# Kernel optimization log

Measured on AMD Instinct MI355X. Metric: run time of the kernel, lower is better.

## Reference

```python
import jax, jax.numpy as jnp
import numpy as np
import math

H = 2048
NH = 16
HD = H // NH  # 128
EPS_LN = 1e-5
RES_SCALE_MAX = 0.3

def _nan_clean(x, lim=10000.0):
    return jnp.nan_to_num(x, nan=0.0, posinf=lim, neginf=-lim)

def setup_inputs() -> dict:
    key = jax.random.key(0)
    ks = jax.random.split(key, 12)
    B, S, T = 4, 2048, 256
    std = 1.0 / math.sqrt(H)
    return {
        "hidden_states": jax.random.normal(ks[0], (B, S, H), jnp.float32),
        "audio_tokens": jax.random.normal(ks[1], (B, T, H), jnp.float32),
        "attention_mask": jax.random.randint(ks[2], (B, T), 0, 2, jnp.int32),
        "Wq": jax.random.normal(ks[3], (H, H), jnp.float32) * std,
        "bq": jnp.zeros((H,), jnp.float32),
        "Wk": jax.random.normal(ks[4], (H, H), jnp.float32) * std,
        "bk": jnp.zeros((H,), jnp.float32),
        "Wv": jax.random.normal(ks[5], (H, H), jnp.float32) * std,
        "bv": jnp.zeros((H,), jnp.float32),
        "Wo": jax.random.normal(ks[6], (H, H), jnp.float32) * std,
        "bo": jnp.zeros((H,), jnp.float32),
        "ln_gamma": jnp.ones((H,), jnp.float32),
        "ln_beta": jnp.zeros((H,), jnp.float32),
        "residual_scale": jnp.float32(0.05),
    }

def reference(hidden_states, audio_tokens, attention_mask,
              Wq, bq, Wk, bk, Wv, bv, Wo, bo, ln_gamma, ln_beta, residual_scale):
    B, S, _ = hidden_states.shape
    T = audio_tokens.shape[1]
    hs = _nan_clean(hidden_states).astype(jnp.float32)
    at = _nan_clean(audio_tokens).astype(jnp.float32)
    # Q/K/V projections -> (B, heads, len, head_dim)
    def proj(x, W, b, L):
        y = x @ W.T + b
        return y.reshape(B, L, NH, HD).transpose(0, 2, 1, 3)
    q = _nan_clean(proj(hs, Wq, bq, S))
    k = _nan_clean(proj(at, Wk, bk, T))
    v = _nan_clean(proj(at, Wv, bv, T))
    scale = max(math.sqrt(HD), 1e-8)
    scores = jnp.einsum('bhsd,bhtd->bhst', q, k) / scale
    scores = jnp.clip(scores, -50.0, 50.0)
    scores = jnp.nan_to_num(scores, nan=0.0, posinf=50.0, neginf=-50.0)
    # mask: int 0/1 -> attend where > 0.5, broadcast (B,1,1,T)
    attend = (attention_mask.astype(jnp.float32) > 0.5)[:, None, None, :]
    scores = jnp.where(attend, scores, -10000.0)
    scores = jnp.clip(scores, -50.0, 50.0)
    probs = jax.nn.softmax(scores, axis=-1)
    probs = jnp.nan_to_num(probs, nan=0.0, posinf=1.0, neginf=0.0)
    probs = probs / (probs.sum(axis=-1, keepdims=True) + 1e-8)
    # dropout: eval mode -> identity
    ctx = jnp.einsum('bhst,bhtd->bhsd', probs, v)
    ctx = ctx.transpose(0, 2, 1, 3).reshape(B, S, H)
    delta = _nan_clean(ctx @ Wo.T + bo)
    rs = jnp.clip(residual_scale, 0.0, RES_SCALE_MAX)
    delta = rs * delta
    # LayerNorm (biased variance, like torch)
    mu = delta.mean(axis=-1, keepdims=True)
    var = jnp.mean((delta - mu) ** 2, axis=-1, keepdims=True)
    delta = (delta - mu) / jnp.sqrt(var + EPS_LN) * ln_gamma + ln_beta
    return delta
```

## Files before the change

kernel.cpp:

```cpp
#include <hip/hip_runtime.h>
#include <stdint.h>

typedef unsigned short u16;
typedef __attribute__((ext_vector_type(8))) __bf16 bf16x8;
typedef __attribute__((ext_vector_type(4))) float f32x4;

#define AS1 __attribute__((address_space(1)))
#define AS3 __attribute__((address_space(3)))

constexpr int HB = 4;
constexpr int SS = 2048;
constexpr int TT = 256;
constexpr int HH = 2048;
constexpr int NHEAD = 16;
constexpr int HD = 128;

__device__ __forceinline__ u16 f2b(float f) {
  union { float f; uint32_t u; } c; c.f = f;
  return (u16)((c.u + 0x7FFFu + ((c.u >> 16) & 1u)) >> 16);
}

__device__ __forceinline__ float b2f(uint32_t lo16) {
  union { uint32_t u; float f; } c; c.u = lo16 << 16;
  return c.f;
}

__global__ __launch_bounds__(256)
void cast_all(const float* __restrict__ hs, const float* __restrict__ at,
              const float* __restrict__ wq, const float* __restrict__ wk,
              const float* __restrict__ wv, const float* __restrict__ wo,
              u16* __restrict__ o_hs, u16* __restrict__ o_at,
              u16* __restrict__ o_wq, u16* __restrict__ o_wk,
              u16* __restrict__ o_wv, u16* __restrict__ o_wo) {
  const int b = blockIdx.x;
  const float* src; u16* dst; int base;
  if (b < 16384)      { src = hs; dst = o_hs; base = 0; }
  else if (b < 18432) { src = at; dst = o_at; base = 16384; }
  else if (b < 22528) { src = wq; dst = o_wq; base = 18432; }
  else if (b < 26624) { src = wk; dst = o_wk; base = 22528; }
  else if (b < 30720) { src = wv; dst = o_wv; base = 26624; }
  else                { src = wo; dst = o_wo; base = 30720; }
  const size_t i = (size_t)(b - base) * 256 + threadIdx.x;
  const float4 v = *(const float4*)(src + i * 4);
  uint2 pk;
  pk.x = (uint32_t)f2b(v.x) | ((uint32_t)f2b(v.y) << 16);
  pk.y = (uint32_t)f2b(v.z) | ((uint32_t)f2b(v.w) << 16);
  *(uint2*)(dst + i * 4) = pk;
}

template<int MODE>
__global__ __launch_bounds__(512, 2)
void gemm8(const u16* __restrict__ A, const u16* __restrict__ Bw,
           const float* __restrict__ bias, const float* __restrict__ rsp,
           void* __restrict__ outp) {
  constexpr int KD = 2048, NT = 64;
  constexpr int BUF = 16384;
  __shared__ u16 lds[4 * BUF];
  const int tid = threadIdx.x;
  const int wv = tid >> 6, ln = tid & 63;
  const int lq = ln >> 4, lr = ln & 15;
  const int wm = wv >> 2, wn = wv & 3;

  const int linb = blockIdx.y * 8 + blockIdx.x;
  const int ns = (linb & 7) * 32 + (linb >> 3);
  const int m0 = (ns >> 3) * 256;
  const int n0 = (ns & 7) * 256;

  int gOff[2];
#pragma unroll
  for (int c = 0; c < 2; ++c) {
    const int g = c * 512 + tid, sr = g >> 3, s = g & 7, l = s ^ (sr & 7);
    gOff[c] = (2 * sr + (l >> 2)) * KD + (l & 3) * 8;
  }
  const u16* Abase = A + (size_t)m0 * KD;
  const u16* Bbase = Bw + (size_t)n0 * KD;

  int aoff[8], boff[4];
#pragma unroll
  for (int m = 0; m < 8; ++m) {
    const int R = wm * 128 + m * 16 + lr, sr = R >> 1;
    aoff[m] = sr * 64 + ((((R & 1) << 2) + lq) ^ (sr & 7)) * 8;
  }
#pragma unroll
  for (int j = 0; j < 4; ++j) {
    const int R = wn * 64 + j * 16 + lr, sr = R >> 1;
    boff[j] = 8192 + sr * 64 + ((((R & 1) << 2) + lq) ^ (sr & 7)) * 8;
  }

#define STAGE_A(c, k0, buf)                                                      \
  __builtin_amdgcn_global_load_lds((AS1 const void*)(Abase + (k0) + gOff[c]),    \
      (AS3 void*)(lds + (buf) * BUF + ((c) * 512 + wv * 64) * 8), 16, 0, 0)
#define STAGE_B(c, k0, buf)                                                      \
  __builtin_amdgcn_global_load_lds((AS1 const void*)(Bbase + (k0) + gOff[c]),    \
      (AS3 void*)(lds + (buf) * BUF + 8192 + ((c) * 512 + wv * 64) * 8), 16, 0, 0)

  f32x4 acc[8][4];
#pragma unroll
  for (int i = 0; i < 8; ++i)
#pragma unroll
    for (int j = 0; j < 4; ++j) acc[i][j] = (f32x4){0.f, 0.f, 0.f, 0.f};

  STAGE_A(0, 0, 0);  STAGE_A(1, 0, 0);  STAGE_B(0, 0, 0);  STAGE_B(1, 0, 0);
  STAGE_A(0, 32, 1); STAGE_A(1, 32, 1); STAGE_B(0, 32, 1); STAGE_B(1, 32, 1);
  STAGE_A(0, 64, 2); STAGE_A(1, 64, 2); STAGE_B(0, 64, 2); STAGE_B(1, 64, 2);
  asm volatile("s_waitcnt vmcnt(8)" ::: "memory");
  __builtin_amdgcn_s_barrier();
  __builtin_amdgcn_sched_barrier(0);

  bf16x8 af[4], bf[4], afn[4];
#pragma unroll
  for (int j = 0; j < 4; ++j) bf[j] = *(const bf16x8*)(lds + boff[j]);
#pragma unroll
  for (int m = 0; m < 4; ++m) af[m] = *(const bf16x8*)(lds + aoff[m]);
  __builtin_amdgcn_sched_barrier(0);

  for (int t = 0; t < NT; ++t) {
    const u16* bb = lds + (t & 3) * BUF;
    const u16* bn = lds + ((t + 1) & 3) * BUF;
    const int stg = (t + 3) & 3;
    const int k3 = (t + 3) * 32;
    const bool doStage = (t + 3) < NT;

#pragma unroll
    for (int m = 0; m < 4; ++m) afn[m] = *(const bf16x8*)(bb + aoff[4 + m]);
    if (doStage) { STAGE_A(0, k3, stg); STAGE_A(1, k3, stg); }
    asm volatile("s_waitcnt lgkmcnt(4)" ::: "memory");
    __builtin_amdgcn_sched_barrier(0);
    __builtin_amdgcn_s_setprio(1);
#pragma unroll
    for (int m = 0; m < 4; ++m)
#pragma unroll
      for (int j = 0; j < 4; ++j)
        acc[m][j] = __builtin_amdgcn_mfma_f32_16x16x32_bf16(af[m], bf[j], acc[m][j], 0, 0, 0);
    __builtin_amdgcn_s_setprio(0);
    if (doStage) { STAGE_B(0, k3, stg); STAGE_B(1, k3, stg); }
    if (t < NT - 3)       asm volatile("s_waitcnt vmcnt(8)" ::: "memory");
    else if (t == NT - 3) asm volatile("s_waitcnt vmcnt(4)" ::: "memory");
    else                  asm volatile("s_waitcnt vmcnt(0)" ::: "memory");
    asm volatile("s_waitcnt lgkmcnt(0)" ::: "memory");
    __builtin_amdgcn_s_barrier();
    __builtin_amdgcn_sched_barrier(0);
    if (t + 1 < NT) {
#pragma unroll
      for (int m = 0; m < 4; ++m) af[m] = *(const bf16x8*)(bn + aoff[m]);
    }
    __builtin_amdgcn_s_setprio(1);
#pragma unroll
    for (int m = 0; m < 4; ++m)
#pragma unroll
      for (int j = 0; j < 4; ++j)
        acc[4 + m][j] = __builtin_amdgcn_mfma_f32_16x16x32_bf16(afn[m], bf[j], acc[4 + m][j], 0, 0, 0);
    __builtin_amdgcn_s_setprio(0);
    if (t + 1 < NT) {
#pragma unroll
      for (int j = 0; j < 4; ++j) bf[j] = *(const bf16x8*)(bn + boff[j]);
    }
    __builtin_amdgcn_sched_barrier(0);
  }
#undef STAGE_A
#undef STAGE_B

  float bj[4];
#pragma unroll
  for (int j = 0; j < 4; ++j) bj[j] = bias[n0 + wn * 64 + j * 16 + lr];
  float rsv = 0.f;
  if constexpr (MODE == 2 || MODE == 3) rsv = fminf(fmaxf(rsp[0], 0.0f), 0.3f);

#pragma unroll
  for (int i = 0; i < 8; ++i)
#pragma unroll
    for (int j = 0; j < 4; ++j)
#pragma unroll
      for (int r = 0; r < 4; ++r) {
        const int row = m0 + wm * 128 + i * 16 + lq * 4 + r;
        const int col = n0 + wn * 64 + j * 16 + lr;
        const float v = acc[i][j][r] + bj[j];
        if constexpr (MODE == 0) {
          ((u16*)outp)[(size_t)row * 2048 + col] = f2b(v);
        } else if constexpr (MODE == 2) {
          ((float*)outp)[(size_t)row * 2048 + col] = v * rsv;
        } else {
          ((u16*)outp)[(size_t)row * 2048 + col] = f2b(v * rsv);
        }
      }
}

__global__ __launch_bounds__(256, 2)
void gemm_kv(const u16* __restrict__ A, const u16* __restrict__ Wk,
             const u16* __restrict__ Wv, const float* __restrict__ bkp,
             const float* __restrict__ bvp, u16* __restrict__ Ko,
             u16* __restrict__ Vto) {
  constexpr int KD = 2048, NT = 64;
  constexpr int BUFE = 8192;
  __shared__ u16 lds[4 * BUFE];
  const bool isV = blockIdx.z != 0;
  const u16* Bw = isV ? Wv : Wk;
  const float* bias = isV ? bvp : bkp;
  const int tid = threadIdx.x;
  const int wave = tid >> 6, lane = tid & 63;
  const int lq = lane >> 4, lr = lane & 15;
  const int wr = wave >> 1, wc = wave & 1;
  const int m0 = blockIdx.y * 128, n0 = blockIdx.x * 128;

  int gOff[2];
#pragma unroll
  for (int c = 0; c < 2; ++c) {
    const int g = c * 256 + tid, sr = g >> 3, s = g & 7, l = s ^ (sr & 7);
    gOff[c] = (2 * sr + (l >> 2)) * KD + (l & 3) * 8;
  }
  const u16* Abase = A + (size_t)m0 * KD;
  const u16* Bbase = Bw + (size_t)n0 * KD;

  int aoff[4], boff[4];
#pragma unroll
  for (int i = 0; i < 4; ++i) {
    const int R = wr * 64 + i * 16 + lr, sr = R >> 1;
    aoff[i] = sr * 64 + ((((R & 1) << 2) + lq) ^ (sr & 7)) * 8;
  }
#pragma unroll
  for (int j = 0; j < 4; ++j) {
    const int R = wc * 64 + j * 16 + lr, sr = R >> 1;
    boff[j] = 4096 + sr * 64 + ((((R & 1) << 2) + lq) ^ (sr & 7)) * 8;
  }

#define KV_STAGE(t3, buf)                                                         \
  {                                                                               \
    _Pragma("unroll")                                                             \
    for (int c_ = 0; c_ < 2; ++c_) {                                              \
      __builtin_amdgcn_global_load_lds(                                           \
          (AS1 const void*)(Abase + (t3) * 32 + gOff[c_]),                        \
          (AS3 void*)(lds + (buf) * BUFE + (c_ * 256 + wave * 64) * 8), 16, 0, 0);\
      __builtin_amdgcn_global_load_lds(                                           \
          (AS1 const void*)(Bbase + (t3) * 32 + gOff[c_]),                        \
          (AS3 void*)(lds + (buf) * BUFE + 4096 + (c_ * 256 + wave * 64) * 8),    \
          16, 0, 0);                                                              \
    }                                                                             \
  }

  f32x4 acc[4][4];
#pragma unroll
  for (int i = 0; i < 4; ++i)
#pragma unroll
    for (int j = 0; j < 4; ++j) acc[i][j] = (f32x4){0.f, 0.f, 0.f, 0.f};

  KV_STAGE(0, 0); KV_STAGE(1, 1); KV_STAGE(2, 2);
  asm volatile("s_waitcnt vmcnt(8)" ::: "memory");
  __builtin_amdgcn_s_barrier();
  __builtin_amdgcn_sched_barrier(0);

  bf16x8 af[4], bfr[4];
#pragma unroll
  for (int i = 0; i < 4; ++i) af[i] = *(const bf16x8*)(lds + aoff[i]);
#pragma unroll
  for (int j = 0; j < 4; ++j) bfr[j] = *(const bf16x8*)(lds + boff[j]);
  __builtin_amdgcn_sched_barrier(0);

  for (int t = 0; t < NT; ++t) {
    if (t + 3 < NT) KV_STAGE(t + 3, (t + 3) & 3);
    asm volatile("s_waitcnt lgkmcnt(0)" ::: "memory");
    __builtin_amdgcn_sched_barrier(0);
    __builtin_amdgcn_s_setprio(1);
#pragma unroll
    for (int i = 0; i < 4; ++i)
#pragma unroll
      for (int j = 0; j < 4; ++j)
        acc[i][j] = __builtin_amdgcn_mfma_f32_16x16x32_bf16(af[i], bfr[j], acc[i][j], 0, 0, 0);
    __builtin_amdgcn_s_setprio(0);
    if (t < NT - 3)       asm volatile("s_waitcnt vmcnt(8)" ::: "memory");
    else if (t == NT - 3) asm volatile("s_waitcnt vmcnt(4)" ::: "memory");
    else                  asm volatile("s_waitcnt vmcnt(0)" ::: "memory");
    __builtin_amdgcn_s_barrier();
    __builtin_amdgcn_sched_barrier(0);
    if (t + 1 < NT) {
      const u16* bn = lds + ((t + 1) & 3) * BUFE;
#pragma unroll
      for (int i = 0; i < 4; ++i) af[i] = *(const bf16x8*)(bn + aoff[i]);
#pragma unroll
      for (int j = 0; j < 4; ++j) bfr[j] = *(const bf16x8*)(bn + boff[j]);
    }
    __builtin_amdgcn_sched_barrier(0);
  }
#undef KV_STAGE

  float bj[4];
#pragma unroll
  for (int j = 0; j < 4; ++j) bj[j] = bias[n0 + wc * 64 + j * 16 + lr];

#pragma unroll
  for (int i = 0; i < 4; ++i)
#pragma unroll
    for (int j = 0; j < 4; ++j)
#pragma unroll
      for (int r = 0; r < 4; ++r) {
        const int row = m0 + wr * 64 + i * 16 + lq * 4 + r;
        const int col = n0 + wc * 64 + j * 16 + lr;
        const float v = acc[i][j][r] + bj[j];
        if (!isV) {
          Ko[(size_t)row * 2048 + col] = f2b(v);
        } else {
          Vto[(size_t)(row >> 8) * (2048 * 256) + (size_t)col * 256 + (row & 255)] = f2b(v);
        }
      }
}

__global__ __launch_bounds__(512, 4)
void attn_kernel(const u16* __restrict__ Q, const u16* __restrict__ Kb,
                 const u16* __restrict__ Vt, const int* __restrict__ mask,
                 u16* __restrict__ ctx) {
  __shared__ u16 sK[2][64 * 128];
  __shared__ u16 sVt[2][128 * 64];
  __shared__ u16 sP[8 * 16 * 64];

  const int tid = threadIdx.x;
  const int wv = tid >> 6, ln = tid & 63;
  const int lq = ln >> 4, lr = ln & 15;
  const int h = blockIdx.y, b = blockIdx.z;
  const int s0blk = blockIdx.x * 128;
  u16* sPw = sP + wv * (16 * 64);

  uint32_t mbits = 0;
#pragma unroll
  for (int g = 0; g < 16; ++g)
    mbits |= (mask[b * TT + g * 16 + lr] != 0 ? 1u : 0u) << g;

  bf16x8 qf[4];
  {
    const u16* qp = Q + ((size_t)b * SS + s0blk + wv * 16 + lr) * HH + (size_t)h * HD + lq * 8;
#pragma unroll
    for (int kd = 0; kd < 4; ++kd) qf[kd] = *(const bf16x8*)(qp + kd * 32);
  }

#define STAGE_KV(c)                                                                      \
  {                                                                                      \
    const int buf_ = (c) & 1;                                                            \
    _Pragma("unroll")                                                                    \
    for (int it = 0; it < 2; ++it) {                                                     \
      const int ub = it * 512 + wv * 64;                                                 \
      const int u = ub + ln;                                                             \
      const int row = u >> 4, slot = u & 15, src = slot ^ (row & 15);                    \
      const u16* g = Kb + ((size_t)b * TT + (c) * 64 + row) * HH + h * HD + src * 8;     \
      __builtin_amdgcn_global_load_lds((AS1 const void*)g,                               \
          (AS3 void*)(sK[buf_] + (size_t)ub * 8), 16, 0, 0);                             \
    }                                                                                    \
    _Pragma("unroll")                                                                    \
    for (int it = 0; it < 2; ++it) {                                                     \
      const int ub = it * 512 + wv * 64;                                                 \
      const int u = ub + ln;                                                             \
      const int row = u >> 3, slot = u & 7, src = slot ^ (row & 7);                      \
      const u16* g = Vt + ((size_t)b * HH + h * HD + row) * TT + (c) * 64 + src * 8;     \
      __builtin_amdgcn_global_load_lds((AS1 const void*)g,                               \
          (AS3 void*)(sVt[buf_] + (size_t)ub * 8), 16, 0, 0);                            \
    }                                                                                    \
  }
  STAGE_KV(0);
  STAGE_KV(1);

  const float scale = 0.08838834764831845f;
  float ls[4] = {0.f, 0.f, 0.f, 0.f};
  f32x4 o[8];
#pragma unroll
  for (int d0 = 0; d0 < 8; ++d0) o[d0] = (f32x4){0.f, 0.f, 0.f, 0.f};

  const int qrow = wv * 16 + lr;
  const int shsrc = ((lr >> 2) << 4) + lr;

  for (int c = 0; c < 4; ++c) {
    const int buf = c & 1;
    if (c < 3) asm volatile("s_waitcnt vmcnt(4)" ::: "memory");
    else       asm volatile("s_waitcnt vmcnt(0)" ::: "memory");
    __syncthreads();

    f32x4 sc[4];
#pragma unroll
    for (int tt = 0; tt < 4; ++tt) {
      f32x4 a = (f32x4){0.f, 0.f, 0.f, 0.f};
#pragma unroll
      for (int kd = 0; kd < 4; ++kd) {
        bf16x8 kf = *(const bf16x8*)(sK[buf] + (size_t)(tt * 16 + lr) * 128 + (size_t)((kd * 4 + lq) ^ lr) * 8);
        a = __builtin_amdgcn_mfma_f32_16x16x32_bf16(qf[kd], kf, a, 0, 0, 0);
      }
      sc[tt] = a;
    }

#pragma unroll
    for (int tt = 0; tt < 4; ++tt) {
      const bool on = (mbits >> (c * 4 + tt)) & 1;
#pragma unroll
      for (int r = 0; r < 4; ++r) {
        float v = sc[tt][r] * scale;
        v = fminf(fmaxf(v, -50.f), 50.f);
        v = on ? v : -50.f;
        const float p = __expf(v);
        sc[tt][r] = p;
        ls[r] += p;
      }
    }

#pragma unroll
    for (int tt = 0; tt < 4; ++tt)
#pragma unroll
      for (int r = 0; r < 4; ++r) {
        const int q = lq * 4 + r;
        const int slot = (tt * 2 + (lr >> 3)) ^ ((q >> 1) & 7);
        sPw[(size_t)q * 64 + slot * 8 + (lr & 7)] = f2b(sc[tt][r]);
      }

    bf16x8 pf[2];
#pragma unroll
    for (int kt = 0; kt < 2; ++kt) {
      const int slot = (kt * 4 + lq) ^ ((lr >> 1) & 7);
      pf[kt] = *(const bf16x8*)(sPw + (size_t)lr * 64 + slot * 8);
    }

#pragma unroll
    for (int d0 = 0; d0 < 8; ++d0)
#pragma unroll
      for (int kt = 0; kt < 2; ++kt) {
        bf16x8 vf = *(const bf16x8*)(sVt[buf] + (size_t)(d0 * 16 + lr) * 64 + (size_t)((kt * 4 + lq) ^ (lr & 7)) * 8);
        o[d0] = __builtin_amdgcn_mfma_f32_16x16x32_bf16(vf, pf[kt], o[d0], 0, 0, 0);
      }
    if (c < 2) {
      __syncthreads();
      STAGE_KV(c + 2);
    }
  }
#undef STAGE_KV

#pragma unroll
  for (int d = 1; d < 16; d <<= 1)
#pragma unroll
    for (int r = 0; r < 4; ++r) ls[r] += __shfl_xor(ls[r], d);

  const float i0 = __shfl(1.0f / ls[0], shsrc), i1 = __shfl(1.0f / ls[1], shsrc);
  const float i2 = __shfl(1.0f / ls[2], shsrc), i3 = __shfl(1.0f / ls[3], shsrc);
  const int rsel = lr & 3;
  const float iq = rsel == 0 ? i0 : rsel == 1 ? i1 : rsel == 2 ? i2 : i3;

  const size_t cbase = ((size_t)b * SS + s0blk + wv * 16 + lr) * HH + (size_t)h * HD;
#pragma unroll
  for (int d0 = 0; d0 < 8; ++d0) {
    uint2 w;
    w.x = (uint32_t)f2b(o[d0][0] * iq) | ((uint32_t)f2b(o[d0][1] * iq) << 16);
    w.y = (uint32_t)f2b(o[d0][2] * iq) | ((uint32_t)f2b(o[d0][3] * iq) << 16);
    *(uint2*)(ctx + cbase + d0 * 16 + lq * 4) = w;
  }
}

__global__ __launch_bounds__(256)
void ln_kernel(const u16* __restrict__ in, float* __restrict__ out,
               const float* __restrict__ gamma, const float* __restrict__ beta) {
  const int row = blockIdx.x, tid = threadIdx.x;
  const u16* x = in + (size_t)row * 2048;
  const uint4 raw = *(const uint4*)(x + tid * 8);
  float xv[8];
  xv[0] = b2f(raw.x & 0xFFFFu); xv[1] = b2f(raw.x >> 16);
  xv[2] = b2f(raw.y & 0xFFFFu); xv[3] = b2f(raw.y >> 16);
  xv[4] = b2f(raw.z & 0xFFFFu); xv[5] = b2f(raw.z >> 16);
  xv[6] = b2f(raw.w & 0xFFFFu); xv[7] = b2f(raw.w >> 16);
  float s = 0.f, ss = 0.f;
#pragma unroll
  for (int i = 0; i < 8; ++i) { s += xv[i]; ss += xv[i] * xv[i]; }
#pragma unroll
  for (int d = 1; d < 64; d <<= 1) {
    s += __shfl_xor(s, d);
    ss += __shfl_xor(ss, d);
  }
  __shared__ float rbuf[8];
  const int w = tid >> 6;
  if ((tid & 63) == 0) { rbuf[w] = s; rbuf[4 + w] = ss; }
  __syncthreads();
  s = rbuf[0] + rbuf[1] + rbuf[2] + rbuf[3];
  ss = rbuf[4] + rbuf[5] + rbuf[6] + rbuf[7];
  const float mu = s * (1.0f / 2048.0f);
  const float var = ss * (1.0f / 2048.0f) - mu * mu;
  const float inv = rsqrtf(var + 1e-5f);
  const float4 g0 = *(const float4*)(gamma + tid * 8);
  const float4 g1 = *(const float4*)(gamma + tid * 8 + 4);
  const float4 b0 = *(const float4*)(beta + tid * 8);
  const float4 b1 = *(const float4*)(beta + tid * 8 + 4);
  float4 y0, y1;
  y0.x = (xv[0] - mu) * inv * g0.x + b0.x;
  y0.y = (xv[1] - mu) * inv * g0.y + b0.y;
  y0.z = (xv[2] - mu) * inv * g0.z + b0.z;
  y0.w = (xv[3] - mu) * inv * g0.w + b0.w;
  y1.x = (xv[4] - mu) * inv * g1.x + b1.x;
  y1.y = (xv[5] - mu) * inv * g1.y + b1.y;
  y1.z = (xv[6] - mu) * inv * g1.z + b1.z;
  y1.w = (xv[7] - mu) * inv * g1.w + b1.w;
  float* o = out + (size_t)row * 2048 + tid * 8;
  *(float4*)o = y0;
  *(float4*)(o + 4) = y1;
}

extern "C" void kernel_launch(void* const* d_in, const int* in_sizes, int n_in,
                              void* d_out, int out_size, void* d_ws, size_t ws_size,
                              hipStream_t stream) {
  (void)in_sizes; (void)n_in; (void)out_size; (void)ws_size;
  const float* hs = (const float*)d_in[0];
  const float* at = (const float*)d_in[1];
  const int* mask = (const int*)d_in[2];
  const float* Wq = (const float*)d_in[3];
  const float* bq = (const float*)d_in[4];
  const float* Wk = (const float*)d_in[5];
  const float* bk = (const float*)d_in[6];
  const float* Wv = (const float*)d_in[7];
  const float* bv = (const float*)d_in[8];
  const float* Wo = (const float*)d_in[9];
  const float* bo = (const float*)d_in[10];
  const float* lg = (const float*)d_in[11];
  const float* lb = (const float*)d_in[12];
  const float* rs = (const float*)d_in[13];

  u16* hs_bf = (u16*)d_ws;
  u16* at_bf = hs_bf + 16777216;
  u16* Wq_bf = at_bf + 2097152;
  u16* Wk_bf = Wq_bf + 4194304;
  u16* Wv_bf = Wk_bf + 4194304;
  u16* Wo_bf = Wv_bf + 4194304;
  u16* Q_bf  = Wo_bf + 4194304;
  u16* K_bf  = Q_bf + 16777216;
  u16* Vt_bf = K_bf + 2097152;
  u16* ctx_bf = hs_bf;
  u16* delta_bf = Q_bf;

  cast_all<<<34816, 256, 0, stream>>>(hs, at, Wq, Wk, Wv, Wo,
                                      hs_bf, at_bf, Wq_bf, Wk_bf, Wv_bf, Wo_bf);

  gemm8<0><<<dim3(8, 32), 512, 0, stream>>>(hs_bf, Wq_bf, bq, nullptr, Q_bf);
  gemm_kv<<<dim3(16, 8, 2), 256, 0, stream>>>(at_bf, Wk_bf, Wv_bf, bk, bv, K_bf, Vt_bf);

  attn_kernel<<<dim3(16, 16, 4), 512, 0, stream>>>(Q_bf, K_bf, Vt_bf, mask, ctx_bf);

  gemm8<3><<<dim3(8, 32), 512, 0, stream>>>(ctx_bf, Wo_bf, bo, rs, delta_bf);
  ln_kernel<<<8192, 256, 0, stream>>>(delta_bf, (float*)d_out, lg, lb);
}
```

Before: 248.8 us.

## Restructure GEMM main loop with double-buffered B fragments and post-barrier staging

Rewrites the bf16 MFMA GEMM inner loop as a two-way unrolled SLICE macro. B fragments now live in two register sets (bf/bfn), so the next tile's B and A loads from LDS are interleaved between the two MFMA halves. All four global-to-LDS stage loads for tile t+3 are now issued together after the barrier. The loop now does a full vmcnt(0) wait every iteration, which shortens how far global prefetch runs ahead. The two-way unroll also assumes the K-tile count NT is even.

```diff
diff --git a/kernel.cpp b/kernel.cpp
--- a/kernel.cpp
+++ b/kernel.cpp
@@ -103,60 +103,72 @@
   STAGE_A(0, 0, 0);  STAGE_A(1, 0, 0);  STAGE_B(0, 0, 0);  STAGE_B(1, 0, 0);
   STAGE_A(0, 32, 1); STAGE_A(1, 32, 1); STAGE_B(0, 32, 1); STAGE_B(1, 32, 1);
   STAGE_A(0, 64, 2); STAGE_A(1, 64, 2); STAGE_B(0, 64, 2); STAGE_B(1, 64, 2);
-  asm volatile("s_waitcnt vmcnt(8)" ::: "memory");
+  asm volatile("s_waitcnt vmcnt(4)" ::: "memory");
   __builtin_amdgcn_s_barrier();
   __builtin_amdgcn_sched_barrier(0);
 
-  bf16x8 af[4], bf[4], afn[4];
+  bf16x8 af[4], afn[4], bf[4], bfn[4];
 #pragma unroll
   for (int j = 0; j < 4; ++j) bf[j] = *(const bf16x8*)(lds + boff[j]);
 #pragma unroll
   for (int m = 0; m < 4; ++m) af[m] = *(const bf16x8*)(lds + aoff[m]);
+#pragma unroll
+  for (int m = 0; m < 4; ++m) afn[m] = *(const bf16x8*)(lds + aoff[4 + m]);
   __builtin_amdgcn_sched_barrier(0);
 
-  for (int t = 0; t < NT; ++t) {
-    const u16* bb = lds + (t & 3) * BUF;
-    const u16* bn = lds + ((t + 1) & 3) * BUF;
-    const int stg = (t + 3) & 3;
-    const int k3 = (t + 3) * 32;
-    const bool doStage = (t + 3) < NT;
-
-#pragma unroll
-    for (int m = 0; m < 4; ++m) afn[m] = *(const bf16x8*)(bb + aoff[4 + m]);
-    if (doStage) { STAGE_A(0, k3, stg); STAGE_A(1, k3, stg); }
-    asm volatile("s_waitcnt lgkmcnt(4)" ::: "memory");
-    __builtin_amdgcn_sched_barrier(0);
-    __builtin_amdgcn_s_setprio(1);
-#pragma unroll
-    for (int m = 0; m < 4; ++m)
-#pragma unroll
-      for (int j = 0; j < 4; ++j)
-        acc[m][j] = __builtin_amdgcn_mfma_f32_16x16x32_bf16(af[m], bf[j], acc[m][j], 0, 0, 0);
-    __builtin_amdgcn_s_setprio(0);
-    if (doStage) { STAGE_B(0, k3, stg); STAGE_B(1, k3, stg); }
-    if (t < NT - 3)       asm volatile("s_waitcnt vmcnt(8)" ::: "memory");
-    else if (t == NT - 3) asm volatile("s_waitcnt vmcnt(4)" ::: "memory");
-    else                  asm volatile("s_waitcnt vmcnt(0)" ::: "memory");
-    asm volatile("s_waitcnt lgkmcnt(0)" ::: "memory");
-    __builtin_amdgcn_s_barrier();
-    __builtin_amdgcn_sched_barrier(0);
-    if (t + 1 < NT) {
-#pragma unroll
-      for (int m = 0; m < 4; ++m) af[m] = *(const bf16x8*)(bn + aoff[m]);
-    }
-    __builtin_amdgcn_s_setprio(1);
-#pragma unroll
-    for (int m = 0; m < 4; ++m)
-#pragma unroll
-      for (int j = 0; j < 4; ++j)
-        acc[4 + m][j] = __builtin_amdgcn_mfma_f32_16x16x32_bf16(afn[m], bf[j], acc[4 + m][j], 0, 0, 0);
-    __builtin_amdgcn_s_setprio(0);
-    if (t + 1 < NT) {
-#pragma unroll
-      for (int j = 0; j < 4; ++j) bf[j] = *(const bf16x8*)(bn + boff[j]);
-    }
-    __builtin_amdgcn_sched_barrier(0);
-  }
+#define SLICE(t, A0, A1, BC, BN)                                                 \
+  {                                                                              \
+    const bool nx = (t) + 1 < NT;                                                \
+    const u16* nb = lds + (((t) + 1) & 3) * BUF;                                 \
+    if (nx) {                                                                    \
+      _Pragma("unroll")                                                          \
+      for (int j = 0; j < 4; ++j) BN[j] = *(const bf16x8*)(nb + boff[j]);        \
+    }                                                                            \
+    __builtin_amdgcn_sched_barrier(0);                                           \
+    __builtin_amdgcn_s_setprio(1);                                               \
+    _Pragma("unroll")                                                            \
+    for (int m = 0; m < 4; ++m)                                                  \
+      _Pragma("unroll")                                                          \
+      for (int j = 0; j < 4; ++j)                                                \
+        acc[m][j] = __builtin_amdgcn_mfma_f32_16x16x32_bf16(A0[m], BC[j], acc[m][j], 0, 0, 0); \
+    __builtin_amdgcn_s_setprio(0);                                               \
+    __builtin_amdgcn_sched_barrier(0);                                           \
+    if (nx) {                                                                    \
+      _Pragma("unroll")                                                          \
+      for (int m = 0; m < 4; ++m) A0[m] = *(const bf16x8*)(nb + aoff[m]);        \
+    }                                                                            \
+    __builtin_amdgcn_sched_barrier(0);                                           \
+    __builtin_amdgcn_s_setprio(1);                                               \
+    _Pragma("unroll")                                                            \
+    for (int m = 0; m < 4; ++m)                                                  \
+      _Pragma("unroll")                                                          \
+      for (int j = 0; j < 4; ++j)                                                \
+        acc[4 + m][j] = __builtin_amdgcn_mfma_f32_16x16x32_bf16(A1[m], BC[j], acc[4 + m][j], 0, 0, 0); \
+    __builtin_amdgcn_s_setprio(0);                                               \
+    __builtin_amdgcn_sched_barrier(0);                                           \
+    if (nx) {                                                                    \
+      _Pragma("unroll")                                                          \
+      for (int m = 0; m < 4; ++m) A1[m] = *(const bf16x8*)(nb + aoff[4 + m]);    \
+      asm volatile("s_waitcnt lgkmcnt(4)" ::: "memory");      \
+    } else {                                                                     \
+      asm volatile("s_waitcnt lgkmcnt(0)" ::: "memory");                         \
+    }                                                                            \
+    asm volatile("s_waitcnt vmcnt(0)" ::: "memory");      \
+    __builtin_amdgcn_s_barrier();                                                \
+    __builtin_amdgcn_sched_barrier(0);                                           \
+    if ((t) + 3 < NT) {                                                          \
+      const int k3 = ((t) + 3) * 32, sb = ((t) + 3) & 3;                         \
+      STAGE_A(0, k3, sb); STAGE_A(1, k3, sb);                                    \
+      STAGE_B(0, k3, sb); STAGE_B(1, k3, sb);                                    \
+    }                                                                            \
+    __builtin_amdgcn_sched_barrier(0);                                           \
+  }
+
+  for (int t = 0; t < NT; t += 2) {
+    SLICE(t, af, afn, bf, bfn);
+    SLICE(t + 1, af, afn, bfn, bf);
+  }
+#undef SLICE
 #undef STAGE_A
 #undef STAGE_B
 
```

After: 258.2 us. 1.04x slower.

## Shrink Q/O projection GEMM tiles to 128x128 with 4-wave blocks

Applied to the files above, without the earlier changes.

The large Q and output-projection GEMMs move from 256x256 tiles on 8-wave blocks to 128x128 tiles on 4-wave blocks, giving 1024 workgroups instead of 256. The split A-fragment double-issue schedule is replaced by a simpler single MFMA phase per k-step, with combined A/B staging. The aim is more blocks for better CU occupancy and load balance on MI355X. The cost is lower arithmetic intensity per tile (more global/LDS traffic per FLOP) and less intra-iteration overlap of LDS reads with MFMA.

```diff
diff --git a/kernel.cpp b/kernel.cpp
--- a/kernel.cpp
+++ b/kernel.cpp
@@ -49,131 +49,117 @@
 }
 
 template<int MODE>
-__global__ __launch_bounds__(512, 2)
+__global__ __launch_bounds__(256, 2)
 void gemm8(const u16* __restrict__ A, const u16* __restrict__ Bw,
            const float* __restrict__ bias, const float* __restrict__ rsp,
            void* __restrict__ outp) {
   constexpr int KD = 2048, NT = 64;
-  constexpr int BUF = 16384;
-  __shared__ u16 lds[4 * BUF];
+  constexpr int BUFE = 8192;
+  __shared__ u16 lds[4 * BUFE];
   const int tid = threadIdx.x;
-  const int wv = tid >> 6, ln = tid & 63;
-  const int lq = ln >> 4, lr = ln & 15;
-  const int wm = wv >> 2, wn = wv & 3;
-
-  const int linb = blockIdx.y * 8 + blockIdx.x;
-  const int ns = (linb & 7) * 32 + (linb >> 3);
-  const int m0 = (ns >> 3) * 256;
-  const int n0 = (ns & 7) * 256;
+  const int wave = tid >> 6, lane = tid & 63;
+  const int lq = lane >> 4, lr = lane & 15;
+  const int wr = wave >> 1, wc = wave & 1;
+
+  const int linb = blockIdx.y * 16 + blockIdx.x;
+  const int ns = (linb & 7) * 128 + (linb >> 3);
+  const int m0 = (ns >> 4) * 128;
+  const int n0 = (ns & 15) * 128;
 
   int gOff[2];
 #pragma unroll
   for (int c = 0; c < 2; ++c) {
-    const int g = c * 512 + tid, sr = g >> 3, s = g & 7, l = s ^ (sr & 7);
+    const int g = c * 256 + tid, sr = g >> 3, s = g & 7, l = s ^ (sr & 7);
     gOff[c] = (2 * sr + (l >> 2)) * KD + (l & 3) * 8;
   }
   const u16* Abase = A + (size_t)m0 * KD;
   const u16* Bbase = Bw + (size_t)n0 * KD;
 
-  int aoff[8], boff[4];
-#pragma unroll
-  for (int m = 0; m < 8; ++m) {
-    const int R = wm * 128 + m * 16 + lr, sr = R >> 1;
-    aoff[m] = sr * 64 + ((((R & 1) << 2) + lq) ^ (sr & 7)) * 8;
+  int aoff[4], boff[4];
+#pragma unroll
+  for (int i = 0; i < 4; ++i) {
+    const int R = wr * 64 + i * 16 + lr, sr = R >> 1;
+    aoff[i] = sr * 64 + ((((R & 1) << 2) + lq) ^ (sr & 7)) * 8;
   }
 #pragma unroll
   for (int j = 0; j < 4; ++j) {
-    const int R = wn * 64 + j * 16 + lr, sr = R >> 1;
-    boff[j] = 8192 + sr * 64 + ((((R & 1) << 2) + lq) ^ (sr & 7)) * 8;
-  }
-
-#define STAGE_A(c, k0, buf)                                                      \
-  __builtin_amdgcn_global_load_lds((AS1 const void*)(Abase + (k0) + gOff[c]),    \
-      (AS3 void*)(lds + (buf) * BUF + ((c) * 512 + wv * 64) * 8), 16, 0, 0)
-#define STAGE_B(c, k0, buf)                                                      \
-  __builtin_amdgcn_global_load_lds((AS1 const void*)(Bbase + (k0) + gOff[c]),    \
-      (AS3 void*)(lds + (buf) * BUF + 8192 + ((c) * 512 + wv * 64) * 8), 16, 0, 0)
-
-  f32x4 acc[8][4];
-#pragma unroll
-  for (int i = 0; i < 8; ++i)
+    const int R = wc * 64 + j * 16 + lr, sr = R >> 1;
+    boff[j] = 4096 + sr * 64 + ((((R & 1) << 2) + lq) ^ (sr & 7)) * 8;
+  }
+
+#define G_STAGE(t3, buf)                                                          \
+  {                                                                               \
+    _Pragma("unroll")                                                             \
+    for (int c_ = 0; c_ < 2; ++c_) {                                              \
+      __builtin_amdgcn_global_load_lds(                                           \
+          (AS1 const void*)(Abase + (t3) * 32 + gOff[c_]),                        \
+          (AS3 void*)(lds + (buf) * BUFE + (c_ * 256 + wave * 64) * 8), 16, 0, 0);\
+      __builtin_amdgcn_global_load_lds(                                           \
+          (AS1 const void*)(Bbase + (t3) * 32 + gOff[c_]),                        \
+          (AS3 void*)(lds + (buf) * BUFE + 4096 + (c_ * 256 + wave * 64) * 8),    \
+          16, 0, 0);                                                              \
+    }                                                                             \
+  }
+
+  f32x4 acc[4][4];
+#pragma unroll
+  for (int i = 0; i < 4; ++i)
 #pragma unroll
     for (int j = 0; j < 4; ++j) acc[i][j] = (f32x4){0.f, 0.f, 0.f, 0.f};
 
-  STAGE_A(0, 0, 0);  STAGE_A(1, 0, 0);  STAGE_B(0, 0, 0);  STAGE_B(1, 0, 0);
-  STAGE_A(0, 32, 1); STAGE_A(1, 32, 1); STAGE_B(0, 32, 1); STAGE_B(1, 32, 1);
-  STAGE_A(0, 64, 2); STAGE_A(1, 64, 2); STAGE_B(0, 64, 2); STAGE_B(1, 64, 2);
+  G_STAGE(0, 0); G_STAGE(1, 1); G_STAGE(2, 2);
   asm volatile("s_waitcnt vmcnt(8)" ::: "memory");
   __builtin_amdgcn_s_barrier();
   __builtin_amdgcn_sched_barrier(0);
 
-  bf16x8 af[4], bf[4], afn[4];
-#pragma unroll
-  for (int j = 0; j < 4; ++j) bf[j] = *(const bf16x8*)(lds + boff[j]);
-#pragma unroll
-  for (int m = 0; m < 4; ++m) af[m] = *(const bf16x8*)(lds + aoff[m]);
+  bf16x8 af[4], bfr[4];
+#pragma unroll
+  for (int i = 0; i < 4; ++i) af[i] = *(const bf16x8*)(lds + aoff[i]);
+#pragma unroll
+  for (int j = 0; j < 4; ++j) bfr[j] = *(const bf16x8*)(lds + boff[j]);
   __builtin_amdgcn_sched_barrier(0);
 
   for (int t = 0; t < NT; ++t) {
-    const u16* bb = lds + (t & 3) * BUF;
-    const u16* bn = lds + ((t + 1) & 3) * BUF;
-    const int stg = (t + 3) & 3;
-    const int k3 = (t + 3) * 32;
-    const bool doStage = (t + 3) < NT;
-
-#pragma unroll
-    for (int m = 0; m < 4; ++m) afn[m] = *(const bf16x8*)(bb + aoff[4 + m]);
-    if (doStage) { STAGE_A(0, k3, stg); STAGE_A(1, k3, stg); }
-    asm volatile("s_waitcnt lgkmcnt(4)" ::: "memory");
+    if (t + 3 < NT) G_STAGE(t + 3, (t + 3) & 3);
+    asm volatile("s_waitcnt lgkmcnt(0)" ::: "memory");
     __builtin_amdgcn_sched_barrier(0);
     __builtin_amdgcn_s_setprio(1);
 #pragma unroll
-    for (int m = 0; m < 4; ++m)
+    for (int i = 0; i < 4; ++i)
 #pragma unroll
       for (int j = 0; j < 4; ++j)
-        acc[m][j] = __builtin_amdgcn_mfma_f32_16x16x32_bf16(af[m], bf[j], acc[m][j], 0, 0, 0);
+        acc[i][j] = __builtin_amdgcn_mfma_f32_16x16x32_bf16(af[i], bfr[j], acc[i][j], 0, 0, 0);
     __builtin_amdgcn_s_setprio(0);
-    if (doStage) { STAGE_B(0, k3, stg); STAGE_B(1, k3, stg); }
     if (t < NT - 3)       asm volatile("s_waitcnt vmcnt(8)" ::: "memory");
     else if (t == NT - 3) asm volatile("s_waitcnt vmcnt(4)" ::: "memory");
     else                  asm volatile("s_waitcnt vmcnt(0)" ::: "memory");
-    asm volatile("s_waitcnt lgkmcnt(0)" ::: "memory");
     __builtin_amdgcn_s_barrier();
     __builtin_amdgcn_sched_barrier(0);
     if (t + 1 < NT) {
-#pragma unroll
-      for (int m = 0; m < 4; ++m) af[m] = *(const bf16x8*)(bn + aoff[m]);
-    }
-    __builtin_amdgcn_s_setprio(1);
-#pragma unroll
-    for (int m = 0; m < 4; ++m)
-#pragma unroll
-      for (int j = 0; j < 4; ++j)
-        acc[4 + m][j] = __builtin_amdgcn_mfma_f32_16x16x32_bf16(afn[m], bf[j], acc[4 + m][j], 0, 0, 0);
-    __builtin_amdgcn_s_setprio(0);
-    if (t + 1 < NT) {
-#pragma unroll
-      for (int j = 0; j < 4; ++j) bf[j] = *(const bf16x8*)(bn + boff[j]);
+      const u16* bn = lds + ((t + 1) & 3) * BUFE;
+#pragma unroll
+      for (int i = 0; i < 4; ++i) af[i] = *(const bf16x8*)(bn + aoff[i]);
+#pragma unroll
+      for (int j = 0; j < 4; ++j) bfr[j] = *(const bf16x8*)(bn + boff[j]);
     }
     __builtin_amdgcn_sched_barrier(0);
   }
-#undef STAGE_A
-#undef STAGE_B
+#undef G_STAGE
 
   float bj[4];
 #pragma unroll
-  for (int j = 0; j < 4; ++j) bj[j] = bias[n0 + wn * 64 + j * 16 + lr];
+  for (int j = 0; j < 4; ++j) bj[j] = bias[n0 + wc * 64 + j * 16 + lr];
   float rsv = 0.f;
   if constexpr (MODE == 2 || MODE == 3) rsv = fminf(fmaxf(rsp[0], 0.0f), 0.3f);
 
 #pragma unroll
-  for (int i = 0; i < 8; ++i)
+  for (int i = 0; i < 4; ++i)
 #pragma unroll
     for (int j = 0; j < 4; ++j)
 #pragma unroll
       for (int r = 0; r < 4; ++r) {
-        const int row = m0 + wm * 128 + i * 16 + lq * 4 + r;
-        const int col = n0 + wn * 64 + j * 16 + lr;
+        const int row = m0 + wr * 64 + i * 16 + lq * 4 + r;
+        const int col = n0 + wc * 64 + j * 16 + lr;
         const float v = acc[i][j][r] + bj[j];
         if constexpr (MODE == 0) {
           ((u16*)outp)[(size_t)row * 2048 + col] = f2b(v);
@@ -361,7 +347,6 @@
 #pragma unroll
   for (int d0 = 0; d0 < 8; ++d0) o[d0] = (f32x4){0.f, 0.f, 0.f, 0.f};
 
-  const int qrow = wv * 16 + lr;
   const int shsrc = ((lr >> 2) << 4) + lr;
 
   for (int c = 0; c < 4; ++c) {
@@ -526,11 +511,11 @@
   cast_all<<<34816, 256, 0, stream>>>(hs, at, Wq, Wk, Wv, Wo,
                                       hs_bf, at_bf, Wq_bf, Wk_bf, Wv_bf, Wo_bf);
 
-  gemm8<0><<<dim3(8, 32), 512, 0, stream>>>(hs_bf, Wq_bf, bq, nullptr, Q_bf);
+  gemm8<0><<<dim3(16, 64), 256, 0, stream>>>(hs_bf, Wq_bf, bq, nullptr, Q_bf);
   gemm_kv<<<dim3(16, 8, 2), 256, 0, stream>>>(at_bf, Wk_bf, Wv_bf, bk, bv, K_bf, Vt_bf);
 
   attn_kernel<<<dim3(16, 16, 4), 512, 0, stream>>>(Q_bf, K_bf, Vt_bf, mask, ctx_bf);
 
-  gemm8<3><<<dim3(8, 32), 512, 0, stream>>>(ctx_bf, Wo_bf, bo, rs, delta_bf);
+  gemm8<3><<<dim3(16, 64), 256, 0, stream>>>(ctx_bf, Wo_bf, bo, rs, delta_bf);
   ln_kernel<<<8192, 256, 0, stream>>>(delta_bf, (float*)d_out, lg, lb);
 }
```

Result: slower. 287.2 us (+15.4%).
